# Optimization experiments

Measured on AMD Instinct MI355X. Metric: run time of the kernel, lower is better.

## Reference

```python
import jax, jax.numpy as jnp
import numpy as np

MARGIN = 1.0
REL_W = 0.3


def setup_inputs() -> dict:
    key = jax.random.key(0)
    ks = jax.random.split(key, 12)
    D = 256
    inp = {
        'support': jax.random.normal(ks[0], (16, 5, 1, 2, D), jnp.float32),
        'support_negative': jax.random.normal(ks[1], (16, 5, 1, 2, D), jnp.float32),
        'query': jax.random.normal(ks[2], (16, 128, 1, 2, D), jnp.float32),
        'negative': jax.random.normal(ks[3], (16, 128, 1, 2, D), jnp.float32),
        # PatternLearner conv weights (kaiming-ish scale), squeezed to 2-D since all convs are (1,3)/(1,1)
        'w1': jax.random.normal(ks[4], (128, 3), jnp.float32) * np.float32(np.sqrt(2.0 / 3.0)),
        'b1': jnp.zeros((128,), jnp.float32),
        'w2': jax.random.normal(ks[5], (64, 128), jnp.float32) * np.float32(np.sqrt(2.0 / 128.0)),
        'b2': jnp.zeros((64,), jnp.float32),
        'w3': jax.random.normal(ks[6], (32, 64), jnp.float32) * np.float32(np.sqrt(2.0 / 64.0)),
        'b3': jnp.zeros((32,), jnp.float32),
        'w4': jax.random.normal(ks[7], (1, 32), jnp.float32) * np.float32(np.sqrt(2.0 / 32.0)),
        'b4': jnp.zeros((1,), jnp.float32),
    }
    return inp


def _pattern_learner(x, w1, b1, w2, b2, w3, b3, w4, b4):
    # x: [B, N, 1, 3, D] -> torch does view+transpose -> conv2d(1,3) over the length-3 axis,
    # then 1x1 channel convs; equivalent to per-(n,d) contractions.
    h = x[:, :, 0]                                   # [B, N, 3, D]
    h = jnp.einsum('bnld,ol->bndo', h, w1) + b1      # [B, N, D, 128]
    h = jax.nn.relu(h)
    h = jax.nn.relu(jnp.einsum('bndi,oi->bndo', h, w2) + b2)
    h = jax.nn.relu(jnp.einsum('bndi,oi->bndo', h, w3) + b3)
    h = jnp.einsum('bndi,oi->bndo', h, w4) + b4      # [B, N, D, 1]
    return h[..., 0]                                 # [B, N, D]


def _concat_relation(pairs, rel):
    # pairs: [B, N, 1, 2, D]; rel: [B, 1, 1, 1, D]
    B, N, C, _, D = pairs.shape
    head = pairs[:, :, :, 0, :]
    tail = pairs[:, :, :, 1, :]
    relb = jnp.broadcast_to(rel[:, :, :, 0, :], (B, N, C, D))
    # torch cat order (relation, head, tail) then reindex [1,0,2] -> (head, relation, tail)
    return jnp.stack([head, relb, tail], axis=3)     # [B, N, 1, 3, D]


def _pattern_match(q, s):
    # q: [B, Nq, D], s: [B, 1, D] -> -L2 norm
    return -jnp.linalg.norm(q - s, axis=-1)


def reference(support, support_negative, query, negative, w1, b1, w2, b2, w3, b3, w4, b4):
    B, num_q = query.shape[0], query.shape[1]
    num_n = negative.shape[1]
    # get_relation(mean=True): tail - head averaged over the few support pairs
    rel = jnp.mean(support[:, :, :, 1, :] - support[:, :, :, 0, :], axis=1, keepdims=True)
    rel = rel[:, :, :, None, :]                      # [B, 1, 1, 1, D]

    sup_t = _concat_relation(support, rel)
    supn_t = _concat_relation(support_negative, rel)
    qry_t = _concat_relation(query, rel)
    neg_t = _concat_relation(negative, rel)

    pl = lambda x: _pattern_learner(x, w1, b1, w2, b2, w3, b3, w4, b4)
    spt_pos = pl(sup_t)                              # [B, few, D]
    spt_neg = pl(supn_t)                             # [B, num_sn, D]
    qry = pl(jnp.concatenate([qry_t, neg_t], axis=1))  # [B, num_q+num_n, D]

    # aggregator == 'relation': prototypes are per-task means of positive support patterns
    proto = jnp.mean(spt_pos, axis=1)                # [B, D]
    spt_pos_m = proto[:, None, :]                    # [B, 1, D]
    spt_neg_m = jnp.mean(spt_neg, axis=1, keepdims=True)

    qry_pos = _pattern_match(qry, spt_pos_m)         # [B, Nq]
    qry_neg = _pattern_match(qry, spt_neg_m)

    # relation_score (vectorized): mean L2 distance to all OTHER tasks' prototypes, negated
    dists = jnp.linalg.norm(qry[:, :, None, :] - proto[None, None, :, :], axis=-1)  # [B, Nq, B]
    idx = jnp.arange(B)
    self_d = dists[idx, :, idx]                      # [B, Nq]
    relation_score = -(dists.sum(-1) - self_d) / (B - 1)

    # margin loss on the true-query slice
    pos_score = _pattern_match(qry[:, :num_q], spt_pos_m)
    neg_score = _pattern_match(qry[:, :num_q], spt_neg_m)
    pos_ = jnp.mean(pos_score)
    neg_ = jnp.mean(neg_score)
    delta_loss = jnp.maximum(0.0, pos_ - neg_ + MARGIN)

    score = jnp.stack([qry_pos, qry_neg], axis=-1).reshape(-1, 2)
    row = jnp.concatenate([jnp.zeros((num_q,), jnp.int32), jnp.ones((num_n,), jnp.int32)])
    y_query = jnp.broadcast_to(row, (B, num_q + num_n)).reshape(-1)

    delta = qry_pos - qry_neg - REL_W * relation_score  # vbm + relation branch
    p_score = delta[:, :num_q]
    n_score = delta[:, num_q:]
    return (score, y_query, p_score, n_score, delta_loss)
```

## Files before the change

kernel.cpp:

```cpp
#include <hip/hip_runtime.h>
#include <hip/hip_bf16.h>

typedef _Float16 f16;
typedef f16 f16x8 __attribute__((ext_vector_type(8)));
typedef f16 f16x2 __attribute__((ext_vector_type(2)));
typedef float f32x4 __attribute__((ext_vector_type(4)));
typedef unsigned int u32;

#define MFMA16(a, b, c) __builtin_amdgcn_mfma_f32_16x16x32_f16((a), (b), (c), 0, 0, 0)

__device__ __forceinline__ u32 pkrz(float a, float b) {
    auto r = __builtin_amdgcn_cvt_pkrtz(a, b);
    return __builtin_bit_cast(u32, r);
}
__device__ __forceinline__ u32 pkmax0(u32 x) {
    f16x2 h = __builtin_bit_cast(f16x2, x);
    f16x2 z = {(f16)0.f, (f16)0.f};
    f16x2 m = __builtin_elementwise_max(h, z);
    return __builtin_bit_cast(u32, m);
}
__device__ __forceinline__ u32 pkrelu(float a, float b) {
    return pkmax0(pkrz(a, b));
}

union U8 { f16x8 h; u32 w[4]; };

#define OFF_REL    0
#define OFF_Y      4096
#define OFF_PROTO  1093632
#define OFF_SNEG   1097728
#define OFF_W      1101828

__global__ void k_prep(const float* __restrict__ sup, const float* __restrict__ supn,
                       const float* __restrict__ w1, const float* __restrict__ b1,
                       const float* __restrict__ w2, const float* __restrict__ w3,
                       const float* __restrict__ w4, float* __restrict__ ws)
{
    int tid = threadIdx.x;
    if (blockIdx.x < 16) {
        int idx = blockIdx.x * 256 + tid;
        int b = idx >> 8, d = idx & 255;
        float acc = 0.f;
        #pragma unroll
        for (int n = 0; n < 5; n++) {
            const float* base = sup + ((b * 5 + n) * 2) * 256 + d;
            acc += base[256] - base[0];
        }
        ws[OFF_REL + idx] = acc * 0.2f;
    } else {
        f16* wf = (f16*)(ws + OFF_W);
        for (int id = tid; id < 29 * 64; id += 256) {
            int frag = id >> 6, lane = id & 63;
            int g = lane >> 4, cr = lane & 15, kb = g * 8;
            float vals[8];
            if (frag < 8) {
                int out = frag * 16 + cr;
                #pragma unroll
                for (int i = 0; i < 8; i++) {
                    int k = kb + i;
                    vals[i] = (k < 3) ? w1[out * 3 + k] : (k == 3 ? b1[out] : 0.f);
                }
            } else if (frag < 24) {
                int f = frag - 8; int t = f >> 2, kk = f & 3; int out = t * 16 + cr;
                #pragma unroll
                for (int i = 0; i < 8; i++) {
                    int u = (2 * kk + (i >> 2)) * 16 + g * 4 + (i & 3);
                    vals[i] = w2[out * 128 + u];
                }
            } else if (frag < 28) {
                int f = frag - 24; int t = f >> 1, kk = f & 1; int out = t * 16 + cr;
                #pragma unroll
                for (int i = 0; i < 8; i++) {
                    int u = (2 * kk + (i >> 2)) * 16 + g * 4 + (i & 3);
                    vals[i] = w3[out * 64 + u];
                }
            } else {
                #pragma unroll
                for (int i = 0; i < 8; i++) {
                    int u = (i >> 2) * 16 + g * 4 + (i & 3);
                    vals[i] = (cr == 0) ? w4[u] : 0.f;
                }
            }
            #pragma unroll
            for (int i = 0; i < 8; i++) wf[id * 8 + i] = (f16)vals[i];
        }
    }
}

__global__ __launch_bounds__(256, 3) void k_main(
    const float* __restrict__ sup, const float* __restrict__ supn,
    const float* __restrict__ qry, const float* __restrict__ neg,
    const float* __restrict__ b2p, const float* __restrict__ b3p,
    const float* __restrict__ b4p, float* __restrict__ ws)
{
    __shared__ __align__(16) f16x8 w2lds[16 * 64];
    __shared__ uint2 stage[4][64];
    const float* wsRel = ws + OFF_REL;
    float* wsY = ws + OFF_Y;
    const f16x8* wf = (const f16x8*)(ws + OFF_W);

    int tid = threadIdx.x, wv = tid >> 6, lane = tid & 63;
    int g = lane >> 4, col = lane & 15;
    const f32x4 zero4 = {0.f, 0.f, 0.f, 0.f};

    #pragma unroll
    for (int i = 0; i < 4; i++) {
        int idx = tid + 256 * i;
        w2lds[idx] = wf[8 * 64 + idx];
    }

    f16x8 w1f[8], w3f[4], w4f;
    #pragma unroll
    for (int f = 0; f < 8; f++)  w1f[f] = wf[f * 64 + lane];
    #pragma unroll
    for (int f = 0; f < 4; f++)  w3f[f] = wf[(24 + f) * 64 + lane];
    w4f = wf[28 * 64 + lane];

    f32x4 bias2[4], bias3[2];
    #pragma unroll
    for (int t = 0; t < 4; t++) {
        int o = t * 16 + g * 4;
        bias2[t] = (f32x4){b2p[o], b2p[o + 1], b2p[o + 2], b2p[o + 3]};
    }
    #pragma unroll
    for (int t = 0; t < 2; t++) {
        int o = t * 16 + g * 4;
        bias3[t] = (f32x4){b3p[o], b3p[o + 1], b3p[o + 2], b3p[o + 3]};
    }
    float b4v = b4p[0];

    __syncthreads();

    int base = (blockIdx.x * 4 + wv) * 256;

    for (int it = 0; it < 4; ++it) {
        int e = base + it * 64 + lane;
        const float* hp; int bd;
        if (e < 40960) {
            int e2 = (e < 20480) ? e : e - 20480;
            int b = e2 / 1280; int r = e2 - b * 1280;
            int n = r >> 8, d = r & 255;
            const float* srcp = (e < 20480) ? sup : supn;
            hp = srcp + ((b * 5 + n) * 2) * 256 + d;
            bd = b * 256 + d;
        } else {
            int e2 = e - 40960;
            int b = e2 >> 16, r = e2 & 65535, m = r >> 8, d = r & 255;
            hp = (m < 128) ? (qry + ((b * 128 + m) * 2) * 256 + d)
                           : (neg + ((b * 128 + (m - 128)) * 2) * 256 + d);
            bd = b * 256 + d;
        }
        float x0 = hp[0], x2 = hp[256], x1 = wsRel[bd];
        stage[wv][lane] = make_uint2(pkrz(x0, x1), pkrz(x2, 1.0f));

        #pragma unroll
        for (int j = 0; j < 4; ++j) {
            U8 b1; b1.w[0] = 0u; b1.w[1] = 0u; b1.w[2] = 0u; b1.w[3] = 0u;
            if (g == 0) {
                uint2 s = stage[wv][j * 16 + col];
                b1.w[0] = s.x; b1.w[1] = s.y;
            }

            f32x4 c1[8];
            #pragma unroll
            for (int t = 0; t < 8; t++) c1[t] = MFMA16(w1f[t], b1.h, zero4);

            U8 b2f[4];
            #pragma unroll
            for (int kk = 0; kk < 4; kk++) {
                b2f[kk].w[0] = pkrelu(c1[2 * kk][0],     c1[2 * kk][1]);
                b2f[kk].w[1] = pkrelu(c1[2 * kk][2],     c1[2 * kk][3]);
                b2f[kk].w[2] = pkrelu(c1[2 * kk + 1][0], c1[2 * kk + 1][1]);
                b2f[kk].w[3] = pkrelu(c1[2 * kk + 1][2], c1[2 * kk + 1][3]);
            }

            f32x4 c2[4];
            #pragma unroll
            for (int t = 0; t < 4; t++) {
                f32x4 c = bias2[t];
                #pragma unroll
                for (int kk = 0; kk < 4; kk++)
                    c = MFMA16(w2lds[(t * 4 + kk) * 64 + lane], b2f[kk].h, c);
                c2[t] = c;
            }

            U8 b3f[2];
            #pragma unroll
            for (int kk = 0; kk < 2; kk++) {
                b3f[kk].w[0] = pkrelu(c2[2 * kk][0],     c2[2 * kk][1]);
                b3f[kk].w[1] = pkrelu(c2[2 * kk][2],     c2[2 * kk][3]);
                b3f[kk].w[2] = pkrelu(c2[2 * kk + 1][0], c2[2 * kk + 1][1]);
                b3f[kk].w[3] = pkrelu(c2[2 * kk + 1][2], c2[2 * kk + 1][3]);
            }

            f32x4 c3[2];
            #pragma unroll
            for (int t = 0; t < 2; t++) {
                f32x4 c = bias3[t];
                #pragma unroll
                for (int kk = 0; kk < 2; kk++) c = MFMA16(w3f[t * 2 + kk], b3f[kk].h, c);
                c3[t] = c;
            }

            U8 b4f;
            b4f.w[0] = pkrelu(c3[0][0], c3[0][1]);
            b4f.w[1] = pkrelu(c3[0][2], c3[0][3]);
            b4f.w[2] = pkrelu(c3[1][0], c3[1][1]);
            b4f.w[3] = pkrelu(c3[1][2], c3[1][3]);

            f32x4 c4 = MFMA16(w4f, b4f.h, zero4);
            if (lane < 16) wsY[base + it * 64 + j * 16 + lane] = c4[0] + b4v;
        }
    }
}

__global__ void k_means(float* __restrict__ ws)
{
    int idx = blockIdx.x * 256 + threadIdx.x;
    int b = idx >> 8, d = idx & 255;
    const float* y = ws + OFF_Y;
    float sp = 0.f, sn = 0.f;
    #pragma unroll
    for (int n = 0; n < 5; n++) {
        sp += y[b * 1280 + n * 256 + d];
        sn += y[20480 + b * 1280 + n * 256 + d];
    }
    ws[OFF_PROTO + idx] = sp * 0.2f;
    ws[OFF_SNEG + idx] = sn * 0.2f;
}

__global__ __launch_bounds__(256) void k_scores(float* __restrict__ ws, float* __restrict__ out)
{
    int row = blockIdx.x * 4 + (threadIdx.x >> 6);
    int lane = threadIdx.x & 63;
    int b = row >> 8, m = row & 255;
    const float* q = ws + OFF_Y + 40960 + row * 256;
    float q0 = q[lane], q1 = q[lane + 64], q2 = q[lane + 128], q3 = q[lane + 192];

    float s[17];
    #pragma unroll
    for (int c = 0; c < 16; c++) {
        const float* p = ws + OFF_PROTO + c * 256;
        float d0 = q0 - p[lane], d1 = q1 - p[lane + 64];
        float d2 = q2 - p[lane + 128], d3 = q3 - p[lane + 192];
        s[c] = d0 * d0 + d1 * d1 + d2 * d2 + d3 * d3;
    }
    {
        const float* p = ws + OFF_SNEG + b * 256;
        float d0 = q0 - p[lane], d1 = q1 - p[lane + 64];
        float d2 = q2 - p[lane + 128], d3 = q3 - p[lane + 192];
        s[16] = d0 * d0 + d1 * d1 + d2 * d2 + d3 * d3;
    }
    #pragma unroll
    for (int off = 32; off > 0; off >>= 1) {
        #pragma unroll
        for (int c = 0; c < 17; c++) s[c] += __shfl_xor(s[c], off, 64);
    }
    float sumd = 0.f, selfd = 0.f;
    #pragma unroll
    for (int c = 0; c < 16; c++) {
        float dc = sqrtf(s[c]);
        sumd += dc;
        if (c == b) selfd = dc;
    }
    float qpos = -selfd;
    float qneg = -sqrtf(s[16]);
    float relation = -(sumd - selfd) * (1.f / 15.f);
    float delta = qpos - qneg - 0.3f * relation;

    if (lane == 0) {
        out[2 * row] = qpos;
        out[2 * row + 1] = qneg;
        out[8192 + row] = (m < 128) ? 0.f : 1.f;
        if (m < 128) out[12288 + b * 128 + m] = delta;
        else         out[14336 + b * 128 + (m - 128)] = delta;
    }
}

__global__ __launch_bounds__(256) void k_final(float* __restrict__ out)
{
    __shared__ float red[2][256];
    int t = threadIdx.x;
    float sp = 0.f, sn = 0.f;
    #pragma unroll
    for (int i = 0; i < 8; i++) {
        int idx = t + 256 * i;
        int b = idx >> 7, m = idx & 127;
        int row = b * 256 + m;
        sp += out[2 * row];
        sn += out[2 * row + 1];
    }
    red[0][t] = sp; red[1][t] = sn;
    __syncthreads();
    #pragma unroll
    for (int off = 128; off > 0; off >>= 1) {
        if (t < off) { red[0][t] += red[0][t + off]; red[1][t] += red[1][t + off]; }
        __syncthreads();
    }
    if (t == 0) {
        float v = (red[0][0] - red[1][0]) * (1.f / 2048.f) + 1.f;
        out[16384] = fmaxf(v, 0.f);
    }
}

extern "C" void kernel_launch(void* const* d_in, const int* in_sizes, int n_in,
                              void* d_out, int out_size, void* d_ws, size_t ws_size,
                              hipStream_t stream)
{
    const float* sup  = (const float*)d_in[0];
    const float* supn = (const float*)d_in[1];
    const float* qry  = (const float*)d_in[2];
    const float* neg  = (const float*)d_in[3];
    const float* w1   = (const float*)d_in[4];
    const float* b1   = (const float*)d_in[5];
    const float* w2   = (const float*)d_in[6];
    const float* b2   = (const float*)d_in[7];
    const float* w3   = (const float*)d_in[8];
    const float* b3   = (const float*)d_in[9];
    const float* w4   = (const float*)d_in[10];
    const float* b4   = (const float*)d_in[11];
    float* ws  = (float*)d_ws;
    float* out = (float*)d_out;

    k_prep  <<<17,   256, 0, stream>>>(sup, supn, w1, b1, w2, w3, w4, ws);
    k_main  <<<1064, 256, 0, stream>>>(sup, supn, qry, neg, b2, b3, b4, ws);
    k_means <<<16,   256, 0, stream>>>(ws);
    k_scores<<<1024, 256, 0, stream>>>(ws, out);
    k_final <<<1,    256, 0, stream>>>(out);
}
```

Baseline: 137.2 us.

## Fold prep and means kernels into main and scores, pair MFMA chains

Removes the separate prep and means kernel launches. Each main block now packs the f16 weight fragments and the relation vectors it needs into shared memory, and each scores block recomputes the support prototypes into shared memory. The MLP inner loop processes two 16-column tiles at once to interleave independent MFMA chains, and the occupancy hint drops from 3 to 2 blocks. The cost is redundant weight packing and prototype averaging in every block, plus higher register pressure.

```diff
diff --git a/kernel.cpp b/kernel.cpp
--- a/kernel.cpp
+++ b/kernel.cpp
@@ -25,96 +25,97 @@
 
 union U8 { f16x8 h; u32 w[4]; };
 
-#define OFF_REL    0
 #define OFF_Y      4096
-#define OFF_PROTO  1093632
-#define OFF_SNEG   1097728
-#define OFF_W      1101828
-
-__global__ void k_prep(const float* __restrict__ sup, const float* __restrict__ supn,
-                       const float* __restrict__ w1, const float* __restrict__ b1,
-                       const float* __restrict__ w2, const float* __restrict__ w3,
-                       const float* __restrict__ w4, float* __restrict__ ws)
-{
-    int tid = threadIdx.x;
-    if (blockIdx.x < 16) {
-        int idx = blockIdx.x * 256 + tid;
-        int b = idx >> 8, d = idx & 255;
-        float acc = 0.f;
-        #pragma unroll
-        for (int n = 0; n < 5; n++) {
-            const float* base = sup + ((b * 5 + n) * 2) * 256 + d;
-            acc += base[256] - base[0];
-        }
-        ws[OFF_REL + idx] = acc * 0.2f;
-    } else {
-        f16* wf = (f16*)(ws + OFF_W);
-        for (int id = tid; id < 29 * 64; id += 256) {
-            int frag = id >> 6, lane = id & 63;
-            int g = lane >> 4, cr = lane & 15, kb = g * 8;
-            float vals[8];
-            if (frag < 8) {
-                int out = frag * 16 + cr;
-                #pragma unroll
-                for (int i = 0; i < 8; i++) {
-                    int k = kb + i;
-                    vals[i] = (k < 3) ? w1[out * 3 + k] : (k == 3 ? b1[out] : 0.f);
-                }
-            } else if (frag < 24) {
-                int f = frag - 8; int t = f >> 2, kk = f & 3; int out = t * 16 + cr;
-                #pragma unroll
-                for (int i = 0; i < 8; i++) {
-                    int u = (2 * kk + (i >> 2)) * 16 + g * 4 + (i & 3);
-                    vals[i] = w2[out * 128 + u];
-                }
-            } else if (frag < 28) {
-                int f = frag - 24; int t = f >> 1, kk = f & 1; int out = t * 16 + cr;
-                #pragma unroll
-                for (int i = 0; i < 8; i++) {
-                    int u = (2 * kk + (i >> 2)) * 16 + g * 4 + (i & 3);
-                    vals[i] = w3[out * 64 + u];
-                }
-            } else {
-                #pragma unroll
-                for (int i = 0; i < 8; i++) {
-                    int u = (i >> 2) * 16 + g * 4 + (i & 3);
-                    vals[i] = (cr == 0) ? w4[u] : 0.f;
-                }
-            }
-            #pragma unroll
-            for (int i = 0; i < 8; i++) wf[id * 8 + i] = (f16)vals[i];
-        }
-    }
-}
-
-__global__ __launch_bounds__(256, 3) void k_main(
+
+__device__ __forceinline__ int b_of(int e) {
+    if (e < 20480) return e / 1280;
+    if (e < 40960) return (e - 20480) / 1280;
+    return (e - 40960) >> 16;
+}
+
+__global__ __launch_bounds__(256, 2) void k_main(
     const float* __restrict__ sup, const float* __restrict__ supn,
     const float* __restrict__ qry, const float* __restrict__ neg,
-    const float* __restrict__ b2p, const float* __restrict__ b3p,
-    const float* __restrict__ b4p, float* __restrict__ ws)
+    const float* __restrict__ w1, const float* __restrict__ b1p,
+    const float* __restrict__ w2, const float* __restrict__ w3,
+    const float* __restrict__ w4, const float* __restrict__ b2p,
+    const float* __restrict__ b3p, const float* __restrict__ b4p,
+    float* __restrict__ ws)
 {
     __shared__ __align__(16) f16x8 w2lds[16 * 64];
+    __shared__ __align__(16) f16x8 wpk[13 * 64];
     __shared__ uint2 stage[4][64];
-    const float* wsRel = ws + OFF_REL;
+    __shared__ float relb[2][256];
     float* wsY = ws + OFF_Y;
-    const f16x8* wf = (const f16x8*)(ws + OFF_W);
 
     int tid = threadIdx.x, wv = tid >> 6, lane = tid & 63;
     int g = lane >> 4, col = lane & 15;
     const f32x4 zero4 = {0.f, 0.f, 0.f, 0.f};
 
+    int blkbase = blockIdx.x * 1024;
+    int rb0 = b_of(blkbase), rb1 = b_of(blkbase + 1023);
+
+    #pragma unroll
+    for (int k = 0; k < 2; k++) {
+        int bb = k ? rb1 : rb0;
+        float acc = 0.f;
+        #pragma unroll
+        for (int n = 0; n < 5; n++) {
+            const float* base = sup + ((bb * 5 + n) * 2) * 256 + tid;
+            acc += base[256] - base[0];
+        }
+        relb[k][tid] = acc * 0.2f;
+    }
+
     #pragma unroll
     for (int i = 0; i < 4; i++) {
-        int idx = tid + 256 * i;
-        w2lds[idx] = wf[8 * 64 + idx];
-    }
+        int id = tid + 256 * i;
+        int f = id >> 6, ln = id & 63;
+        int gg = ln >> 4, cr = ln & 15;
+        int t = f >> 2, kk = f & 3, out = t * 16 + cr;
+        U8 v;
+        #pragma unroll
+        for (int i2 = 0; i2 < 8; i2++) {
+            int u = (2 * kk + (i2 >> 2)) * 16 + gg * 4 + (i2 & 3);
+            v.h[i2] = (f16)w2[out * 128 + u];
+        }
+        w2lds[id] = v.h;
+    }
+    for (int id = tid; id < 13 * 64; id += 256) {
+        int fi = id >> 6, ln = id & 63;
+        int gg = ln >> 4, cr = ln & 15, kb = gg * 8;
+        U8 v;
+        if (fi < 8) {
+            int out = fi * 16 + cr;
+            #pragma unroll
+            for (int i2 = 0; i2 < 8; i2++) {
+                int k = kb + i2;
+                v.h[i2] = (f16)((k < 3) ? w1[out * 3 + k] : (k == 3 ? b1p[out] : 0.f));
+            }
+        } else if (fi < 12) {
+            int f = fi - 8; int t = f >> 1, kk = f & 1; int out = t * 16 + cr;
+            #pragma unroll
+            for (int i2 = 0; i2 < 8; i2++) {
+                int u = (2 * kk + (i2 >> 2)) * 16 + gg * 4 + (i2 & 3);
+                v.h[i2] = (f16)w3[out * 64 + u];
+            }
+        } else {
+            #pragma unroll
+            for (int i2 = 0; i2 < 8; i2++) {
+                int u = (i2 >> 2) * 16 + gg * 4 + (i2 & 3);
+                v.h[i2] = (f16)((cr == 0) ? w4[u] : 0.f);
+            }
+        }
+        wpk[id] = v.h;
+    }
+    __syncthreads();
 
     f16x8 w1f[8], w3f[4], w4f;
     #pragma unroll
-    for (int f = 0; f < 8; f++)  w1f[f] = wf[f * 64 + lane];
-    #pragma unroll
-    for (int f = 0; f < 4; f++)  w3f[f] = wf[(24 + f) * 64 + lane];
-    w4f = wf[28 * 64 + lane];
+    for (int f = 0; f < 8; f++) w1f[f] = wpk[f * 64 + lane];
+    #pragma unroll
+    for (int f = 0; f < 4; f++) w3f[f] = wpk[(8 + f) * 64 + lane];
+    w4f = wpk[12 * 64 + lane];
 
     f32x4 bias2[4], bias3[2];
     #pragma unroll
@@ -129,126 +130,159 @@
     }
     float b4v = b4p[0];
 
-    __syncthreads();
-
-    int base = (blockIdx.x * 4 + wv) * 256;
+    int base = blkbase + wv * 256;
 
     for (int it = 0; it < 4; ++it) {
         int e = base + it * 64 + lane;
-        const float* hp; int bd;
+        const float* hp; int bb, dd;
         if (e < 40960) {
             int e2 = (e < 20480) ? e : e - 20480;
-            int b = e2 / 1280; int r = e2 - b * 1280;
-            int n = r >> 8, d = r & 255;
+            bb = e2 / 1280; int r = e2 - bb * 1280;
+            int n = r >> 8; dd = r & 255;
             const float* srcp = (e < 20480) ? sup : supn;
-            hp = srcp + ((b * 5 + n) * 2) * 256 + d;
-            bd = b * 256 + d;
+            hp = srcp + ((bb * 5 + n) * 2) * 256 + dd;
         } else {
             int e2 = e - 40960;
-            int b = e2 >> 16, r = e2 & 65535, m = r >> 8, d = r & 255;
-            hp = (m < 128) ? (qry + ((b * 128 + m) * 2) * 256 + d)
-                           : (neg + ((b * 128 + (m - 128)) * 2) * 256 + d);
-            bd = b * 256 + d;
-        }
-        float x0 = hp[0], x2 = hp[256], x1 = wsRel[bd];
+            bb = e2 >> 16; int r = e2 & 65535, m = r >> 8; dd = r & 255;
+            hp = (m < 128) ? (qry + ((bb * 128 + m) * 2) * 256 + dd)
+                           : (neg + ((bb * 128 + (m - 128)) * 2) * 256 + dd);
+        }
+        float x0 = hp[0], x2 = hp[256];
+        float x1 = relb[(bb == rb0) ? 0 : 1][dd];
         stage[wv][lane] = make_uint2(pkrz(x0, x1), pkrz(x2, 1.0f));
 
         #pragma unroll
-        for (int j = 0; j < 4; ++j) {
-            U8 b1; b1.w[0] = 0u; b1.w[1] = 0u; b1.w[2] = 0u; b1.w[3] = 0u;
+        for (int jp = 0; jp < 2; ++jp) {
+            U8 b1a, b1b;
+            #pragma unroll
+            for (int q = 0; q < 4; q++) { b1a.w[q] = 0u; b1b.w[q] = 0u; }
             if (g == 0) {
-                uint2 s = stage[wv][j * 16 + col];
-                b1.w[0] = s.x; b1.w[1] = s.y;
-            }
-
-            f32x4 c1[8];
-            #pragma unroll
-            for (int t = 0; t < 8; t++) c1[t] = MFMA16(w1f[t], b1.h, zero4);
-
-            U8 b2f[4];
+                uint2 sa = stage[wv][(2 * jp) * 16 + col];
+                uint2 sb = stage[wv][(2 * jp + 1) * 16 + col];
+                b1a.w[0] = sa.x; b1a.w[1] = sa.y;
+                b1b.w[0] = sb.x; b1b.w[1] = sb.y;
+            }
+
+            f32x4 c1a[8], c1b[8];
+            #pragma unroll
+            for (int t = 0; t < 8; t++) {
+                c1a[t] = MFMA16(w1f[t], b1a.h, zero4);
+                c1b[t] = MFMA16(w1f[t], b1b.h, zero4);
+            }
+
+            U8 b2fa[4], b2fb[4];
             #pragma unroll
             for (int kk = 0; kk < 4; kk++) {
-                b2f[kk].w[0] = pkrelu(c1[2 * kk][0],     c1[2 * kk][1]);
-                b2f[kk].w[1] = pkrelu(c1[2 * kk][2],     c1[2 * kk][3]);
-                b2f[kk].w[2] = pkrelu(c1[2 * kk + 1][0], c1[2 * kk + 1][1]);
-                b2f[kk].w[3] = pkrelu(c1[2 * kk + 1][2], c1[2 * kk + 1][3]);
-            }
-
-            f32x4 c2[4];
+                b2fa[kk].w[0] = pkrelu(c1a[2 * kk][0],     c1a[2 * kk][1]);
+                b2fa[kk].w[1] = pkrelu(c1a[2 * kk][2],     c1a[2 * kk][3]);
+                b2fa[kk].w[2] = pkrelu(c1a[2 * kk + 1][0], c1a[2 * kk + 1][1]);
+                b2fa[kk].w[3] = pkrelu(c1a[2 * kk + 1][2], c1a[2 * kk + 1][3]);
+                b2fb[kk].w[0] = pkrelu(c1b[2 * kk][0],     c1b[2 * kk][1]);
+                b2fb[kk].w[1] = pkrelu(c1b[2 * kk][2],     c1b[2 * kk][3]);
+                b2fb[kk].w[2] = pkrelu(c1b[2 * kk + 1][0], c1b[2 * kk + 1][1]);
+                b2fb[kk].w[3] = pkrelu(c1b[2 * kk + 1][2], c1b[2 * kk + 1][3]);
+            }
+
+            f32x4 c2a[4], c2b[4];
             #pragma unroll
             for (int t = 0; t < 4; t++) {
-                f32x4 c = bias2[t];
+                f32x4 ca = bias2[t], cb = bias2[t];
                 #pragma unroll
-                for (int kk = 0; kk < 4; kk++)
-                    c = MFMA16(w2lds[(t * 4 + kk) * 64 + lane], b2f[kk].h, c);
-                c2[t] = c;
-            }
-
-            U8 b3f[2];
+                for (int kk = 0; kk < 4; kk++) {
+                    f16x8 wfr = w2lds[(t * 4 + kk) * 64 + lane];
+                    ca = MFMA16(wfr, b2fa[kk].h, ca);
+                    cb = MFMA16(wfr, b2fb[kk].h, cb);
+                }
+                c2a[t] = ca; c2b[t] = cb;
+            }
+
+            U8 b3fa[2], b3fb[2];
             #pragma unroll
             for (int kk = 0; kk < 2; kk++) {
-                b3f[kk].w[0] = pkrelu(c2[2 * kk][0],     c2[2 * kk][1]);
-                b3f[kk].w[1] = pkrelu(c2[2 * kk][2],     c2[2 * kk][3]);
-                b3f[kk].w[2] = pkrelu(c2[2 * kk + 1][0], c2[2 * kk + 1][1]);
-                b3f[kk].w[3] = pkrelu(c2[2 * kk + 1][2], c2[2 * kk + 1][3]);
-            }
-
-            f32x4 c3[2];
+                b3fa[kk].w[0] = pkrelu(c2a[2 * kk][0],     c2a[2 * kk][1]);
+                b3fa[kk].w[1] = pkrelu(c2a[2 * kk][2],     c2a[2 * kk][3]);
+                b3fa[kk].w[2] = pkrelu(c2a[2 * kk + 1][0], c2a[2 * kk + 1][1]);
+                b3fa[kk].w[3] = pkrelu(c2a[2 * kk + 1][2], c2a[2 * kk + 1][3]);
+                b3fb[kk].w[0] = pkrelu(c2b[2 * kk][0],     c2b[2 * kk][1]);
+                b3fb[kk].w[1] = pkrelu(c2b[2 * kk][2],     c2b[2 * kk][3]);
+                b3fb[kk].w[2] = pkrelu(c2b[2 * kk + 1][0], c2b[2 * kk + 1][1]);
+                b3fb[kk].w[3] = pkrelu(c2b[2 * kk + 1][2], c2b[2 * kk + 1][3]);
+            }
+
+            f32x4 c3a[2], c3b[2];
             #pragma unroll
             for (int t = 0; t < 2; t++) {
-                f32x4 c = bias3[t];
+                f32x4 ca = bias3[t], cb = bias3[t];
                 #pragma unroll
-                for (int kk = 0; kk < 2; kk++) c = MFMA16(w3f[t * 2 + kk], b3f[kk].h, c);
-                c3[t] = c;
-            }
-
-            U8 b4f;
-            b4f.w[0] = pkrelu(c3[0][0], c3[0][1]);
-            b4f.w[1] = pkrelu(c3[0][2], c3[0][3]);
-            b4f.w[2] = pkrelu(c3[1][0], c3[1][1]);
-            b4f.w[3] = pkrelu(c3[1][2], c3[1][3]);
-
-            f32x4 c4 = MFMA16(w4f, b4f.h, zero4);
-            if (lane < 16) wsY[base + it * 64 + j * 16 + lane] = c4[0] + b4v;
-        }
-    }
-}
-
-__global__ void k_means(float* __restrict__ ws)
-{
-    int idx = blockIdx.x * 256 + threadIdx.x;
-    int b = idx >> 8, d = idx & 255;
-    const float* y = ws + OFF_Y;
-    float sp = 0.f, sn = 0.f;
-    #pragma unroll
-    for (int n = 0; n < 5; n++) {
-        sp += y[b * 1280 + n * 256 + d];
-        sn += y[20480 + b * 1280 + n * 256 + d];
-    }
-    ws[OFF_PROTO + idx] = sp * 0.2f;
-    ws[OFF_SNEG + idx] = sn * 0.2f;
+                for (int kk = 0; kk < 2; kk++) {
+                    ca = MFMA16(w3f[t * 2 + kk], b3fa[kk].h, ca);
+                    cb = MFMA16(w3f[t * 2 + kk], b3fb[kk].h, cb);
+                }
+                c3a[t] = ca; c3b[t] = cb;
+            }
+
+            U8 b4fa, b4fb;
+            b4fa.w[0] = pkrelu(c3a[0][0], c3a[0][1]);
+            b4fa.w[1] = pkrelu(c3a[0][2], c3a[0][3]);
+            b4fa.w[2] = pkrelu(c3a[1][0], c3a[1][1]);
+            b4fa.w[3] = pkrelu(c3a[1][2], c3a[1][3]);
+            b4fb.w[0] = pkrelu(c3b[0][0], c3b[0][1]);
+            b4fb.w[1] = pkrelu(c3b[0][2], c3b[0][3]);
+            b4fb.w[2] = pkrelu(c3b[1][0], c3b[1][1]);
+            b4fb.w[3] = pkrelu(c3b[1][2], c3b[1][3]);
+
+            f32x4 c4a = MFMA16(w4f, b4fa.h, zero4);
+            f32x4 c4b = MFMA16(w4f, b4fb.h, zero4);
+            if (lane < 16) {
+                wsY[base + it * 64 + (2 * jp) * 16 + lane]     = c4a[0] + b4v;
+                wsY[base + it * 64 + (2 * jp + 1) * 16 + lane] = c4b[0] + b4v;
+            }
+        }
+    }
 }
 
 __global__ __launch_bounds__(256) void k_scores(float* __restrict__ ws, float* __restrict__ out)
 {
-    int row = blockIdx.x * 4 + (threadIdx.x >> 6);
-    int lane = threadIdx.x & 63;
-    int b = row >> 8, m = row & 255;
-    const float* q = ws + OFF_Y + 40960 + row * 256;
+    __shared__ float proto[16][256];
+    __shared__ float snegs[256];
+    const float* y = ws + OFF_Y;
+    int tid = threadIdx.x;
+    int row0 = blockIdx.x * 4;
+    int b = row0 >> 8;
+
+    #pragma unroll
+    for (int i = 0; i < 16; i++) {
+        int idx = tid + 256 * i;
+        int c = idx >> 8, d = idx & 255;
+        float s = 0.f;
+        #pragma unroll
+        for (int n = 0; n < 5; n++) s += y[c * 1280 + n * 256 + d];
+        proto[c][d] = s * 0.2f;
+    }
+    {
+        float s = 0.f;
+        #pragma unroll
+        for (int n = 0; n < 5; n++) s += y[20480 + b * 1280 + n * 256 + tid];
+        snegs[tid] = s * 0.2f;
+    }
+    __syncthreads();
+
+    int row = row0 + (tid >> 6);
+    int lane = tid & 63;
+    int m = row & 255;
+    const float* q = y + 40960 + row * 256;
     float q0 = q[lane], q1 = q[lane + 64], q2 = q[lane + 128], q3 = q[lane + 192];
 
     float s[17];
     #pragma unroll
     for (int c = 0; c < 16; c++) {
-        const float* p = ws + OFF_PROTO + c * 256;
-        float d0 = q0 - p[lane], d1 = q1 - p[lane + 64];
-        float d2 = q2 - p[lane + 128], d3 = q3 - p[lane + 192];
+        float d0 = q0 - proto[c][lane],       d1 = q1 - proto[c][lane + 64];
+        float d2 = q2 - proto[c][lane + 128], d3 = q3 - proto[c][lane + 192];
         s[c] = d0 * d0 + d1 * d1 + d2 * d2 + d3 * d3;
     }
     {
-        const float* p = ws + OFF_SNEG + b * 256;
-        float d0 = q0 - p[lane], d1 = q1 - p[lane + 64];
-        float d2 = q2 - p[lane + 128], d3 = q3 - p[lane + 192];
+        float d0 = q0 - snegs[lane],       d1 = q1 - snegs[lane + 64];
+        float d2 = q2 - snegs[lane + 128], d3 = q3 - snegs[lane + 192];
         s[16] = d0 * d0 + d1 * d1 + d2 * d2 + d3 * d3;
     }
     #pragma unroll
@@ -322,9 +356,7 @@
     float* ws  = (float*)d_ws;
     float* out = (float*)d_out;
 
-    k_prep  <<<17,   256, 0, stream>>>(sup, supn, w1, b1, w2, w3, w4, ws);
-    k_main  <<<1064, 256, 0, stream>>>(sup, supn, qry, neg, b2, b3, b4, ws);
-    k_means <<<16,   256, 0, stream>>>(ws);
+    k_main  <<<1064, 256, 0, stream>>>(sup, supn, qry, neg, w1, b1, w2, w3, w4, b2, b3, b4, ws);
     k_scores<<<1024, 256, 0, stream>>>(ws, out);
     k_final <<<1,    256, 0, stream>>>(out);
 }
```

Result: faster. 130.8 us (-4.7%).
